# Performance work log

Measured on AMD Instinct MI355X. Metric: run time of the kernel, lower is better.

Reference implementation:

```python
import jax, jax.numpy as jnp
import numpy as np

B, S, D, H = 4, 2048, 256, 8  # batch, seq, d_hidden (= per-head dim), n_heads
ROPE_BASE = 10000.0


def _rope_tables(seq_len, dim, dtype=jnp.float32):
    # standard RoPE: inv_freq over half the dim, half-split rotate
    inv_freq = 1.0 / (ROPE_BASE ** (jnp.arange(0, dim, 2, dtype=jnp.float32) / dim))
    angles = jnp.arange(seq_len, dtype=jnp.float32)[:, None] * inv_freq[None, :]  # [S, D/2]
    return jnp.cos(angles).astype(dtype), jnp.sin(angles).astype(dtype)


def _apply_rope(x, cos, sin):
    # x: [..., S, D]; cos/sin: [S, D/2]
    d2 = x.shape[-1] // 2
    x1, x2 = x[..., :d2], x[..., d2:]
    return jnp.concatenate([x1 * cos - x2 * sin, x1 * sin + x2 * cos], axis=-1)


def setup_inputs() -> dict:
    key = jax.random.key(0)
    ks = jax.random.split(key, 5)
    scale_in = 1.0 / np.sqrt(D)
    scale_out = 1.0 / np.sqrt(H * D)
    return {
        "x": jax.random.normal(ks[0], (B, S, D), jnp.float32),
        "w_qkv": jax.random.normal(ks[1], (3 * H * D, D), jnp.float32) * scale_in,
        "b_qkv": jax.random.normal(ks[2], (3 * H * D,), jnp.float32) * 0.02,
        "w_out": jax.random.normal(ks[3], (D, H * D), jnp.float32) * scale_out,
        "b_out": jax.random.normal(ks[4], (D,), jnp.float32) * 0.02,
    }


def reference(x, w_qkv, b_qkv, w_out, b_out):
    b, s, d = x.shape
    # QKV projection: [b, s, 3*H*D]
    qkv = x @ w_qkv.T + b_qkv
    # einops '(qkv heads hidden)': qkv axis outermost -> [b, s, 3, H, D]
    qkv = qkv.reshape(b, s, 3, H, D)
    qkv = jnp.transpose(qkv, (2, 0, 3, 1, 4))  # [3, b, H, s, D]
    q, k, v = qkv[0], qkv[1], qkv[2]
    cos, sin = _rope_tables(s, D, x.dtype)
    q = _apply_rope(q, cos, sin)
    k = _apply_rope(k, cos, sin)
    # non-causal SDPA, scale = 1/sqrt(D)
    scores = jnp.einsum('bhqd,bhkd->bhqk', q, k) / jnp.sqrt(jnp.asarray(D, x.dtype))
    probs = jax.nn.softmax(scores, axis=-1)
    attn = jnp.einsum('bhqk,bhkd->bhqd', probs, v)  # [b, H, s, D]
    # '... heads seq hidden -> ... seq (heads hidden)'
    attn_concat = jnp.transpose(attn, (0, 2, 1, 3)).reshape(b, s, H * D)
    out = attn_concat @ w_out.T + b_out
    return x + out
```

## Files before the change

kernel.cpp:

```cpp
#include <hip/hip_runtime.h>
#include <hip/hip_bf16.h>
#include <stdint.h>

#define Sq   2048
#define Dq   256
#define Hq   8
#define NQKV 6144
#define HD   2048
#define MTOK 8192

typedef __attribute__((ext_vector_type(8))) short short8;
typedef __attribute__((ext_vector_type(4))) float f32x4;
typedef __attribute__((ext_vector_type(16))) float f32x16;
typedef __attribute__((ext_vector_type(4))) int i32x4;

__device__ __forceinline__ float bf2f(short v) {
  union { float f; unsigned u; } x; x.u = ((unsigned)(unsigned short)v) << 16; return x.f;
}
__device__ __forceinline__ short f2bf(float f) {
  union { float f; unsigned u; } x; x.f = f;
  unsigned r = x.u + 0x7fffu + ((x.u >> 16) & 1u);
  return (short)(r >> 16);
}
__device__ __forceinline__ unsigned f2e4m3(float f) {
  union { float f; unsigned u; } x; x.f = f;
  unsigned sign = (x.u >> 24) & 0x80u;
  float af = fabsf(f);
  if (af >= 448.f) return sign | 0x7Eu;
  if (af < 0.0009765625f) return sign;
  int e = (int)((x.u >> 23) & 0xff) - 127;
  int L = (e < -6) ? -9 : e - 3;
  union { float f; unsigned u; } s1, s2;
  s1.u = (unsigned)(127 - L) << 23;
  s2.u = (unsigned)(127 + L) << 23;
  float t = rintf(af * s1.f);
  float val = t * s2.f;
  if (val == 0.f) return sign;
  union { float f; unsigned u; } y; y.f = val;
  int e2 = (int)((y.u >> 23) & 0xff) - 127;
  unsigned byte;
  if (e2 < -6) byte = (unsigned)(val * 512.f);
  else byte = ((unsigned)(e2 + 7) << 3) | ((y.u >> 20) & 7u);
  return sign | byte;
}
__device__ __forceinline__ void gload16(const void* g, void* lds) {
  auto g1 = (const __attribute__((address_space(1))) int*)(uintptr_t)g;
  auto l3 = (__attribute__((address_space(3))) int*)(uintptr_t)lds;
  __builtin_amdgcn_global_load_lds(g1, l3, 16, 0, 0);
}
__device__ __forceinline__ float exp2a(float x) {
  float r; asm("v_exp_f32 %0, %1" : "=v"(r) : "v"(x)); return r;
}
__device__ __forceinline__ unsigned cvtpk(float lo, float hi) {
  unsigned r; asm("v_cvt_pk_bf16_f32 %0, %1, %2" : "=v"(r) : "v"(lo), "v"(hi)); return r;
}
__device__ __forceinline__ void plswap(unsigned &a, unsigned &b) {
  asm volatile("v_permlane32_swap_b32 %0, %1" : "+v"(a), "+v"(b));
}
__device__ __forceinline__ f32x16 fz16() {
  f32x16 z;
#pragma unroll
  for (int e = 0; e < 16; e++) z[e] = 0.f;
  return z;
}

__global__ __launch_bounds__(256) void k_prep(
    const float* __restrict__ x, const float* __restrict__ wqkv,
    const float* __restrict__ wout,
    short* __restrict__ xb, short* __restrict__ wqb, short* __restrict__ wob,
    float* __restrict__ cost, float* __restrict__ sint)
{
  long i = (long)blockIdx.x * 256 + threadIdx.x;
  const long n_x  = (long)MTOK * Dq;
  const long n_wq = (long)NQKV * Dq;
  const long n_wo = (long)Dq * HD;
  const long n_tab = (long)Sq * 128;
  if (i < n_x) { xb[i] = f2bf(x[i]); return; }
  i -= n_x;
  if (i < n_wq) { wqb[i] = f2bf(wqkv[i]); return; }
  i -= n_wq;
  if (i < n_wo) { wob[i] = f2bf(wout[i]); return; }
  i -= n_wo;
  if (i < n_tab) {
    int s = (int)(i >> 7), j = (int)(i & 127);
    float inv = __expf(-(float)j * (9.2103403720f / 128.0f));
    float a = (float)s * inv;
    cost[i] = cosf(a);
    sint[i] = sinf(a);
  }
}

template<int EPI, int BN>
__global__ __launch_bounds__(256, 2) void k_gemm(
    const short* __restrict__ A, const short* __restrict__ Bt,
    const float* __restrict__ bias, const float* __restrict__ resid,
    void* __restrict__ Cp, int M, int N, int K)
{
  constexpr int MI = (BN == 128) ? 4 : 2;
  constexpr int WRS = MI * 16;
  constexpr int BROUNDS = BN / 32;
  __shared__ short As[128 * 64];
  __shared__ short Bs[BN * 64];
  const int tid = threadIdx.x;
  const int w = tid >> 6, lane = tid & 63;
  const int grp = lane >> 4, l15 = lane & 15;
  const int wr = (BN == 128) ? (w >> 1) : w;
  const int wc = (BN == 128) ? (w & 1) : 0;
  const int m0 = blockIdx.y * 128, n0 = blockIdx.x * BN;

  f32x4 acc[MI][4];
#pragma unroll
  for (int i = 0; i < MI; i++)
#pragma unroll
    for (int j = 0; j < 4; j++) acc[i][j] = f32x4{0.f, 0.f, 0.f, 0.f};

  for (int kt = 0; kt < K; kt += 64) {
#pragma unroll
    for (int r = 0; r < 4; r++) {
      int G = r * 256 + tid;
      int row = G >> 3, gc = G & 7;
      gload16(A + (size_t)(m0 + row) * K + kt + gc * 8,
              (char*)As + (r * 256 + w * 64) * 16);
    }
#pragma unroll
    for (int r = 0; r < BROUNDS; r++) {
      int G = r * 256 + tid;
      int row = G >> 3, gc = G & 7;
      gload16(Bt + (size_t)(n0 + row) * K + kt + gc * 8,
              (char*)Bs + (r * 256 + w * 64) * 16);
    }
    __syncthreads();
#pragma unroll
    for (int kk = 0; kk < 2; kk++) {
      short8 af[MI], bf[4];
#pragma unroll
      for (int mi = 0; mi < MI; mi++) {
        int row = wr * WRS + mi * 16 + l15;
        af[mi] = *(const short8*)&As[row * 64 + kk * 32 + grp * 8];
      }
#pragma unroll
      for (int ni = 0; ni < 4; ni++) {
        int row = wc * 64 + ni * 16 + l15;
        bf[ni] = *(const short8*)&Bs[row * 64 + kk * 32 + grp * 8];
      }
#pragma unroll
      for (int mi = 0; mi < MI; mi++)
#pragma unroll
        for (int ni = 0; ni < 4; ni++)
          acc[mi][ni] = __builtin_amdgcn_mfma_f32_16x16x32_bf16(
              af[mi], bf[ni], acc[mi][ni], 0, 0, 0);
    }
    __syncthreads();
  }
#pragma unroll
  for (int mi = 0; mi < MI; mi++) {
#pragma unroll
    for (int ni = 0; ni < 4; ni++) {
      int colb = n0 + wc * 64 + ni * 16 + l15;
      float bv = bias[colb];
#pragma unroll
      for (int j = 0; j < 4; j++) {
        int row = m0 + wr * WRS + mi * 16 + grp * 4 + j;
        float v = acc[mi][ni][j] + bv;
        if (EPI == 0) {
          ((short*)Cp)[(size_t)row * N + colb] = f2bf(v);
        } else {
          size_t o = (size_t)row * N + colb;
          ((float*)Cp)[o] = v + resid[o];
        }
      }
    }
  }
}

__global__ __launch_bounds__(256) void k_ropef8(
    short* __restrict__ qkv, const float* __restrict__ cost,
    const float* __restrict__ sint)
{
  int tt = blockIdx.x * 2 + (threadIdx.x >> 7);
  int i = threadIdx.x & 127;
  int h = i >> 4, jv = i & 15;
  int s = tt & (Sq - 1);
  const short* qrow = qkv + (size_t)tt * NQKV + h * 256 + jv * 8;
  short8 q1 = *(const short8*)qrow;
  short8 q2 = *(const short8*)(qrow + 128);
  short8 k1 = *(const short8*)(qrow + 2048);
  short8 k2 = *(const short8*)(qrow + 2048 + 128);
  const float* cp = &cost[(size_t)s * 128 + jv * 8];
  const float* sp = &sint[(size_t)s * 128 + jv * 8];
  unsigned long oq1 = 0, oq2 = 0, ok1 = 0, ok2 = 0;
#pragma unroll
  for (int e = 0; e < 8; e++) {
    float c = cp[e], sn = sp[e];
    float a = bf2f(q1[e]), b2 = bf2f(q2[e]);
    oq1 |= (unsigned long)f2e4m3(a * c - b2 * sn) << (8 * e);
    oq2 |= (unsigned long)f2e4m3(a * sn + b2 * c) << (8 * e);
    float ka = bf2f(k1[e]), kb = bf2f(k2[e]);
    ok1 |= (unsigned long)f2e4m3(ka * c - kb * sn) << (8 * e);
    ok2 |= (unsigned long)f2e4m3(ka * sn + kb * c) << (8 * e);
  }
  __syncthreads();
  char* dst = (char*)qkv + (size_t)tt * 12288 + h * 256 + jv * 8;
  *(unsigned long*)(dst)              = oq1;
  *(unsigned long*)(dst + 128)        = oq2;
  *(unsigned long*)(dst + 2048)       = ok1;
  *(unsigned long*)(dst + 2048 + 128) = ok2;
}

__global__ __launch_bounds__(256) void k_vt(
    const short* __restrict__ qkv, short* __restrict__ vT)
{
  __shared__ short t[64][72];
  int kt = blockIdx.x, dt = blockIdx.y, bh = blockIdx.z;
  int b = bh >> 3, h = bh & 7;
  int tid = threadIdx.x;
  int r = tid >> 2, c0 = (tid & 3) * 16;
  const short* src = &qkv[(size_t)(b * Sq + kt * 64 + r) * NQKV + 4096 + h * 256 + dt * 64 + c0];
  short8 v0 = *(const short8*)src;
  short8 v1 = *(const short8*)(src + 8);
#pragma unroll
  for (int e = 0; e < 8; e++) { t[r][c0 + e] = v0[e]; t[r][c0 + 8 + e] = v1[e]; }
  __syncthreads();
  short8 o0, o1;
#pragma unroll
  for (int e = 0; e < 8; e++) { o0[e] = t[c0 + e][r]; o1[e] = t[c0 + 8 + e][r]; }
  short* dst = &vT[(size_t)(bh * 256 + dt * 64 + r) * Sq + kt * 64 + c0];
  *(short8*)dst = o0;
  *(short8*)(dst + 8) = o1;
}

__global__ __launch_bounds__(256, 2) void k_attn(
    const char* __restrict__ qkvb, const short* __restrict__ vT,
    short* __restrict__ attn)
{
  __shared__ char  Ks[2][8192];
  __shared__ short Vs[2][8192];
  const int tid = threadIdx.x;
  const int w = tid >> 6, lane = tid & 63;
  const int l31 = lane & 31, hi = lane >> 5;
  const int id = blockIdx.x;
  const int bh = (id & 7) * 4 + ((id >> 3) & 3);
  const int qb0 = (id >> 5) * 128;
  const int b = bh >> 3, h = bh & 7;
  const float QS = 0.090168441f;

  long qf[16];
  {
    const char* qbase = qkvb + (size_t)(b * Sq + qb0 + w * 32 + l31) * 12288 + h * 256 + hi * 8;
#pragma unroll
    for (int kc = 0; kc < 16; kc++) qf[kc] = *(const long*)(qbase + kc * 16);
  }
  f32x16 o[8];
#pragma unroll
  for (int dt = 0; dt < 8; dt++) o[dt] = fz16();
  float m = -3e38f, l = 0.f;

  const char* kbase = qkvb + (size_t)(b * Sq) * 12288 + 2048 + h * 256;
  const short* vbase = &vT[(size_t)bh * 256 * Sq];

#pragma unroll
  for (int r = 0; r < 2; r++) {
    int G = r * 256 + tid;
    gload16(kbase + (size_t)(G & 31) * 12288 + (G >> 5) * 16,
            (char*)&Ks[0][0] + (r * 256 + w * 64) * 16);
  }
#pragma unroll
  for (int r = 0; r < 4; r++) {
    int G = r * 256 + tid;
    gload16(vbase + (size_t)(G & 255) * Sq + (G >> 8) * 8,
            (char*)&Vs[0][0] + (r * 256 + w * 64) * 16);
  }
  __syncthreads();

  int cur = 0;
  for (int kt = 0; kt < Sq / 32; kt++) {
    if (kt + 1 < Sq / 32) {
#pragma unroll
      for (int r = 0; r < 2; r++) {
        int G = r * 256 + tid;
        gload16(kbase + (size_t)((kt + 1) * 32 + (G & 31)) * 12288 + (G >> 5) * 16,
                (char*)&Ks[cur ^ 1][0] + (r * 256 + w * 64) * 16);
      }
#pragma unroll
      for (int r = 0; r < 4; r++) {
        int G = r * 256 + tid;
        gload16(vbase + (size_t)(G & 255) * Sq + (kt + 1) * 32 + (G >> 8) * 8,
                (char*)&Vs[cur ^ 1][0] + (r * 256 + w * 64) * 16);
      }
    }

    f32x16 sc = fz16();
    __builtin_amdgcn_s_setprio(1);
#pragma unroll
    for (int kc = 0; kc < 16; kc++) {
      long ka = *(const long*)&Ks[cur][(kc * 32 + l31) * 16 + hi * 8];
      sc = __builtin_amdgcn_mfma_f32_32x32x16_fp8_fp8(ka, qf[kc], sc, 0, 0, 0);
    }
    __builtin_amdgcn_s_setprio(0);

    float t8[8];
#pragma unroll
    for (int e = 0; e < 8; e++) t8[e] = fmaxf(sc[e], sc[e + 8]);
#pragma unroll
    for (int e = 0; e < 4; e++) t8[e] = fmaxf(t8[e], t8[e + 4]);
    t8[0] = fmaxf(t8[0], t8[2]); t8[1] = fmaxf(t8[1], t8[3]);
    float pmax = fmaxf(t8[0], t8[1]);
    pmax = fmaxf(pmax, __shfl_xor(pmax, 32, 64));
    float pms = pmax * QS;
    if (!__all(pms <= m + 8.0f)) {
      float nm = fmaxf(m, pms);
      float f = exp2a(m - nm);
      l *= f;
#pragma unroll
      for (int dt = 0; dt < 8; dt++)
#pragma unroll
        for (int e = 0; e < 16; e++) o[dt][e] *= f;
      m = nm;
    }
#pragma unroll
    for (int e = 0; e < 16; e++) sc[e] = exp2a(fmaf(sc[e], QS, -m));
    float r8[8];
#pragma unroll
    for (int e = 0; e < 8; e++) r8[e] = sc[e] + sc[e + 8];
#pragma unroll
    for (int e = 0; e < 4; e++) r8[e] = r8[e] + r8[e + 4];
    r8[0] += r8[2]; r8[1] += r8[3];
    float rs = r8[0] + r8[1];
    rs += __shfl_xor(rs, 32, 64);
    l += rs;

    short8 pa[2];
    {
      unsigned x0 = cvtpk(sc[0], sc[1]);
      unsigned y0 = cvtpk(sc[4], sc[5]);
      unsigned x1 = cvtpk(sc[2], sc[3]);
      unsigned y1 = cvtpk(sc[6], sc[7]);
      plswap(x0, y0);
      plswap(x1, y1);
      i32x4 w0; w0[0] = x0; w0[1] = x1; w0[2] = y0; w0[3] = y1;
      pa[0] = __builtin_bit_cast(short8, w0);
      unsigned x2 = cvtpk(sc[8],  sc[9]);
      unsigned y2 = cvtpk(sc[12], sc[13]);
      unsigned x3 = cvtpk(sc[10], sc[11]);
      unsigned y3 = cvtpk(sc[14], sc[15]);
      plswap(x2, y2);
      plswap(x3, y3);
      i32x4 w1; w1[0] = x2; w1[1] = x3; w1[2] = y2; w1[3] = y3;
      pa[1] = __builtin_bit_cast(short8, w1);
    }

    __builtin_amdgcn_s_setprio(1);
#pragma unroll
    for (int dt = 0; dt < 8; dt++) {
#pragma unroll
      for (int ks = 0; ks < 2; ks++) {
        short8 vb = *(const short8*)&Vs[cur][(((ks * 2 + hi) << 8) | (dt * 32 + l31)) * 8];
        o[dt] = __builtin_amdgcn_mfma_f32_32x32x16_bf16(pa[ks], vb, o[dt], 0, 0, 0);
      }
    }
    __builtin_amdgcn_s_setprio(0);

    __syncthreads();
    cur ^= 1;
  }

  float linv = 1.0f / l;
  float li[16];
#pragma unroll
  for (int e = 0; e < 16; e++)
    li[e] = __shfl(linv, (e & 3) + 8 * (e >> 2) + 4 * hi, 64);
  short* orow = &attn[(size_t)(b * Sq + qb0 + w * 32) * HD + h * 256 + l31];
#pragma unroll
  for (int dt = 0; dt < 8; dt++)
#pragma unroll
    for (int e = 0; e < 16; e++)
      orow[(size_t)((e & 3) + 8 * (e >> 2) + 4 * hi) * HD + dt * 32] = f2bf(o[dt][e] * li[e]);
}

extern "C" void kernel_launch(void* const* d_in, const int* in_sizes, int n_in,
                              void* d_out, int out_size, void* d_ws, size_t ws_size,
                              hipStream_t stream) {
  const float* x     = (const float*)d_in[0];
  const float* w_qkv = (const float*)d_in[1];
  const float* b_qkv = (const float*)d_in[2];
  const float* w_out = (const float*)d_in[3];
  const float* b_out = (const float*)d_in[4];
  float* out = (float*)d_out;

  char* ws = (char*)d_ws;
  short* qkv  = (short*)ws;
  short* vT   = (short*)(ws + 100663296);
  short* attn = (short*)(ws + 134217728);
  short* xb   = (short*)(ws + 167772160);
  short* wqb  = (short*)(ws + 171966464);
  short* wob  = (short*)(ws + 175112192);
  float* cost = (float*)(ws + 176160768);
  float* sint = (float*)(ws + 177209344);

  k_prep<<<dim3(17408), 256, 0, stream>>>(x, w_qkv, w_out, xb, wqb, wob, cost, sint);
  k_gemm<0, 128><<<dim3(NQKV / 128, MTOK / 128), 256, 0, stream>>>(
      xb, wqb, b_qkv, nullptr, qkv, MTOK, NQKV, Dq);
  k_ropef8<<<dim3(MTOK / 2), 256, 0, stream>>>(qkv, cost, sint);
  k_vt<<<dim3(32, 4, 32), 256, 0, stream>>>(qkv, vT);
  k_attn<<<dim3(512), 256, 0, stream>>>((const char*)qkv, vT, attn);
  k_gemm<1, 64><<<dim3(Dq / 64, MTOK / 128), 256, 0, stream>>>(
      attn, wob, b_out, x, out, MTOK, Dq, HD);
}
```

Baseline: 339.0 us.

## Swizzle GEMM block mapping across XCDs and simplify attention K/V staging pointers

Both GEMMs now use a 1D grid, and the block index is remapped so that consecutive blocks placed on the same XCD share A rows or B columns, which should improve L2 reuse on the multi-XCD MI355X. The attention kernel replaces the per-iteration recomputed K/V load addresses with precomputed pointers that are incremented, to cut integer address arithmetic in the main loop. The block swizzle is hardcoded to these grid sizes (6 column tiles per XCD, and 8 row tiles by 4 column tiles), so it is only correct for these exact shapes.

```diff
diff --git a/kernel.cpp b/kernel.cpp
--- a/kernel.cpp
+++ b/kernel.cpp
@@ -90,7 +90,7 @@
   }
 }
 
-template<int EPI, int BN>
+template<int EPI, int BN, int SWZ>
 __global__ __launch_bounds__(256, 2) void k_gemm(
     const short* __restrict__ A, const short* __restrict__ Bt,
     const float* __restrict__ bias, const float* __restrict__ resid,
@@ -106,7 +106,14 @@
   const int grp = lane >> 4, l15 = lane & 15;
   const int wr = (BN == 128) ? (w >> 1) : w;
   const int wc = (BN == 128) ? (w & 1) : 0;
-  const int m0 = blockIdx.y * 128, n0 = blockIdx.x * BN;
+  int rowb, colb;
+  {
+    int id = blockIdx.x;
+    int xcd = id & 7, idx = id >> 3;
+    if (SWZ == 0) { colb = xcd * 6 + idx % 6; rowb = idx / 6; }
+    else          { rowb = xcd * 8 + (idx >> 2); colb = idx & 3; }
+  }
+  const int m0 = rowb * 128, n0 = colb * BN;
 
   f32x4 acc[MI][4];
 #pragma unroll
@@ -156,16 +163,16 @@
   for (int mi = 0; mi < MI; mi++) {
 #pragma unroll
     for (int ni = 0; ni < 4; ni++) {
-      int colb = n0 + wc * 64 + ni * 16 + l15;
-      float bv = bias[colb];
+      int colc = n0 + wc * 64 + ni * 16 + l15;
+      float bv = bias[colc];
 #pragma unroll
       for (int j = 0; j < 4; j++) {
         int row = m0 + wr * WRS + mi * 16 + grp * 4 + j;
         float v = acc[mi][ni][j] + bv;
         if (EPI == 0) {
-          ((short*)Cp)[(size_t)row * N + colb] = f2bf(v);
+          ((short*)Cp)[(size_t)row * N + colc] = f2bf(v);
         } else {
-          size_t o = (size_t)row * N + colb;
+          size_t o = (size_t)row * N + colc;
           ((float*)Cp)[o] = v + resid[o];
         }
       }
@@ -255,39 +262,24 @@
   for (int dt = 0; dt < 8; dt++) o[dt] = fz16();
   float m = -3e38f, l = 0.f;
 
-  const char* kbase = qkvb + (size_t)(b * Sq) * 12288 + 2048 + h * 256;
-  const short* vbase = &vT[(size_t)bh * 256 * Sq];
-
-#pragma unroll
-  for (int r = 0; r < 2; r++) {
-    int G = r * 256 + tid;
-    gload16(kbase + (size_t)(G & 31) * 12288 + (G >> 5) * 16,
-            (char*)&Ks[0][0] + (r * 256 + w * 64) * 16);
-  }
-#pragma unroll
-  for (int r = 0; r < 4; r++) {
-    int G = r * 256 + tid;
-    gload16(vbase + (size_t)(G & 255) * Sq + (G >> 8) * 8,
-            (char*)&Vs[0][0] + (r * 256 + w * 64) * 16);
-  }
+  const char* kp = qkvb + (size_t)(b * Sq) * 12288 + 2048 + h * 256
+                 + (size_t)(tid & 31) * 12288 + (tid >> 5) * 16;
+  const char* vp = (const char*)&vT[(size_t)bh * 256 * Sq] + (size_t)tid * (Sq * 2);
+
+#define STAGE(BI) { \
+    char* kD = (char*)Ks + (BI) * 8192  + w * 1024; \
+    char* vD = (char*)Vs + (BI) * 16384 + w * 1024; \
+    gload16(kp,       kD);          gload16(kp + 128, kD + 4096); \
+    gload16(vp,       vD);          gload16(vp + 16,  vD + 4096); \
+    gload16(vp + 32,  vD + 8192);   gload16(vp + 48,  vD + 12288); \
+    kp += 32 * 12288; vp += 64; }
+
+  STAGE(0)
   __syncthreads();
 
   int cur = 0;
   for (int kt = 0; kt < Sq / 32; kt++) {
-    if (kt + 1 < Sq / 32) {
-#pragma unroll
-      for (int r = 0; r < 2; r++) {
-        int G = r * 256 + tid;
-        gload16(kbase + (size_t)((kt + 1) * 32 + (G & 31)) * 12288 + (G >> 5) * 16,
-                (char*)&Ks[cur ^ 1][0] + (r * 256 + w * 64) * 16);
-      }
-#pragma unroll
-      for (int r = 0; r < 4; r++) {
-        int G = r * 256 + tid;
-        gload16(vbase + (size_t)(G & 255) * Sq + (kt + 1) * 32 + (G >> 8) * 8,
-                (char*)&Vs[cur ^ 1][0] + (r * 256 + w * 64) * 16);
-      }
-    }
+    if (kt + 1 < Sq / 32) STAGE(cur ^ 1)
 
     f32x16 sc = fz16();
     __builtin_amdgcn_s_setprio(1);
@@ -363,6 +355,7 @@
     __syncthreads();
     cur ^= 1;
   }
+#undef STAGE
 
   float linv = 1.0f / l;
   float li[16];
@@ -398,11 +391,11 @@
   float* sint = (float*)(ws + 177209344);
 
   k_prep<<<dim3(17408), 256, 0, stream>>>(x, w_qkv, w_out, xb, wqb, wob, cost, sint);
-  k_gemm<0, 128><<<dim3(NQKV / 128, MTOK / 128), 256, 0, stream>>>(
+  k_gemm<0, 128, 0><<<dim3(3072), 256, 0, stream>>>(
       xb, wqb, b_qkv, nullptr, qkv, MTOK, NQKV, Dq);
   k_ropef8<<<dim3(MTOK / 2), 256, 0, stream>>>(qkv, cost, sint);
   k_vt<<<dim3(32, 4, 32), 256, 0, stream>>>(qkv, vT);
   k_attn<<<dim3(512), 256, 0, stream>>>((const char*)qkv, vT, attn);
-  k_gemm<1, 64><<<dim3(Dq / 64, MTOK / 128), 256, 0, stream>>>(
+  k_gemm<1, 64, 1><<<dim3(256), 256, 0, stream>>>(
       attn, wob, b_out, x, out, MTOK, Dq, HD);
 }
```

Result: no change. 332.4 us (-2.0%).
